# Kernel tuning notes

Hardware: AMD Instinct MI355X
Metric: run time of the kernel (lower is better)

## Reference

```python
import jax, jax.numpy as jnp
import numpy as np

LAMBDA_COORD = 5.0
LAMBDA_NOOBJ = 0.5
CELL_SILE = 1.0 / 7.0


def setup_inputs() -> dict:
    key = jax.random.key(0)
    k1, k2, k3 = jax.random.split(key, 3)
    B, S, C = 16384, 49, 30
    predictions = jax.random.normal(k1, (B, S, C), dtype=jnp.float32)
    targets = jax.random.uniform(k2, (B, S, C), dtype=jnp.float32)
    # confidence column must be exactly 0/1 for the equality masks in the loss
    obj = (jax.random.uniform(k3, (B, S)) < 0.3).astype(jnp.float32)
    targets = targets.at[:, :, 4].set(obj)
    return {"predictions": predictions, "targets": targets}


def reference(predictions, targets):
    # Flatten cells: row-major order matches torch boolean indexing order.
    p = predictions.reshape(-1, 30)  # [N, 30], N = B*49
    t = targets.reshape(-1, 30)
    conf = t[:, 4]
    coord_mask = conf == 1.0
    noobj = (conf == 0.0).astype(p.dtype)

    # no-object confidence loss on columns [4, 9]
    noobj_loss = LAMBDA_NOOBJ * jnp.sum(
        noobj * ((p[:, 4] - t[:, 4]) ** 2 + (p[:, 9] - t[:, 9]) ** 2))

    # The original zips N_obj rows against N_obj//2 output rows, so only the
    # first floor(N_obj/2) object cells (in flattened order) contribute.
    n_obj = jnp.sum(coord_mask.astype(jnp.int32))
    rank = jnp.cumsum(coord_mask.astype(jnp.int32))  # 1-indexed object rank
    w = (coord_mask & (rank <= n_obj // 2)).astype(p.dtype)

    # pred boxes: columns [0:4] and [5:9] -> [N, 2, 4]
    pb = p[:, :10].reshape(-1, 2, 5)[..., :4]
    # faithful in-place transform: a = xy*c - wh ; b = a*c + wh
    pa = pb[..., :2] * CELL_SILE - pb[..., 2:4]
    pbb = pa * CELL_SILE + pb[..., 2:4]
    pbox = jnp.concatenate([pa, pbb], axis=-1)  # [N, 2, 4]

    tb = jnp.square(t[:, :4])
    ta = tb[:, :2] * CELL_SILE - tb[:, 2:4]
    tbb = ta * CELL_SILE + tb[:, 2:4]
    tbox = jnp.concatenate([ta, tbb], axis=-1)  # [N, 4]

    # torchvision.ops.box_iou, batched over cells
    lt = jnp.maximum(pbox[..., :2], tbox[:, None, :2])
    rb = jnp.minimum(pbox[..., 2:], tbox[:, None, 2:])
    whd = jnp.clip(rb - lt, 0.0)
    inter = whd[..., 0] * whd[..., 1]  # [N, 2]
    area_p = (pbox[..., 2] - pbox[..., 0]) * (pbox[..., 3] - pbox[..., 1])
    area_t = (tbox[:, 2] - tbox[:, 0]) * (tbox[:, 3] - tbox[:, 1])
    iou = inter / (area_p + area_t[:, None] - inter)  # [N, 2]

    idx = jnp.argmax(iou, axis=1)  # responsible box per cell
    sel = jnp.take_along_axis(p[:, :10].reshape(-1, 2, 5),
                              idx[:, None, None], axis=1)[:, 0, :]  # [N, 5]
    obj_idx = jnp.argmax(t[:, 10:], axis=1)
    sel_cls = jnp.take_along_axis(p[:, 10:], obj_idx[:, None], axis=1)[:, 0]

    center = jnp.sum(w * jnp.sum((sel[:, :2] - t[:, :2]) ** 2, axis=1))
    xywh = jnp.sum(w * jnp.sum((sel[:, 2:4] - t[:, 2:4]) ** 2, axis=1))
    # original compares column 5 twice (confidence_loss and classier_loss are
    # the same term): pred class prob vs constant 1
    conf_l = jnp.sum(w * (sel_cls - 1.0) ** 2)
    cls_l = jnp.sum(w * (sel_cls - 1.0) ** 2)

    return LAMBDA_COORD * (center + xywh + conf_l + cls_l) + noobj_loss
```

## Files before the change

kernel.cpp:

```cpp
#include <hip/hip_runtime.h>


#define COLS 30
#define NB   3136

#define ROW_MATH_BODY                                                        \
    const float C = 1.0f / 7.0f;                                             \
    float conf = b2.x;                         \
    coord = (conf == 1.0f);                                                  \
    noo = 0.0f;                                                              \
    if (conf == 0.0f) {                                                      \
        float d4_ = a2.x - conf;                                             \
        float d9_ = a4.y - b4.y;                                             \
        noo = d4_ * d4_ + d9_ * d9_;                                         \
    }                                                                        \
    float T0 = b0.x, T1 = b0.y, T2v = b1.x, T3 = b1.y;                       \
    float tb0 = T0 * T0, tb1 = T1 * T1, tb2 = T2v * T2v, tb3 = T3 * T3;      \
    float tax = tb0 * C - tb2, tay = tb1 * C - tb3;                          \
    float tbx = tax * C + tb2, tby = tay * C + tb3;                          \
    float areaT = (tbx - tax) * (tby - tay);                                 \
    float pax0 = a0.x * C - a1.x, pay0 = a0.y * C - a1.y;                    \
    float pbx0 = pax0 * C + a1.x, pby0 = pay0 * C + a1.y;                    \
    float pax1 = a2.y * C - a3.y, pay1 = a3.x * C - a4.x;                    \
    float pbx1 = pax1 * C + a3.y, pby1 = pay1 * C + a4.x;                    \
    float ltx = fmaxf(pax0, tax), lty = fmaxf(pay0, tay);                    \
    float rbx = fminf(pbx0, tbx), rby = fminf(pby0, tby);                    \
    float wx = fmaxf(rbx - ltx, 0.0f), wy = fmaxf(rby - lty, 0.0f);          \
    float inter = wx * wy;                                                   \
    float areaP = (pbx0 - pax0) * (pby0 - pay0);                             \
    float iou0 = inter / (areaP + areaT - inter);                            \
    ltx = fmaxf(pax1, tax); lty = fmaxf(pay1, tay);                          \
    rbx = fminf(pbx1, tbx); rby = fminf(pby1, tby);                          \
    wx = fmaxf(rbx - ltx, 0.0f); wy = fmaxf(rby - lty, 0.0f);                \
    inter = wx * wy;                                                         \
    areaP = (pbx1 - pax1) * (pby1 - pay1);                                   \
    float iou1 = inter / (areaP + areaT - inter);                            \
    int idx = (iou1 > iou0) ? 1 : 0;              \
    float sx = idx ? a2.y : a0.x;                                            \
    float sy = idx ? a3.x : a0.y;                                            \
    float sw = idx ? a3.y : a1.x;                                            \
    float sh = idx ? a4.x : a1.y;                                            \
    float best = b5.x, pc = a5.x;                \
    CLS_STEP(b5.y,  a5.y)  CLS_STEP(b6.x,  a6.x)  CLS_STEP(b6.y,  a6.y)      \
    CLS_STEP(b7.x,  a7.x)  CLS_STEP(b7.y,  a7.y)  CLS_STEP(b8.x,  a8.x)      \
    CLS_STEP(b8.y,  a8.y)  CLS_STEP(b9.x,  a9.x)  CLS_STEP(b9.y,  a9.y)      \
    CLS_STEP(b10.x, a10.x) CLS_STEP(b10.y, a10.y) CLS_STEP(b11.x, a11.x)     \
    CLS_STEP(b11.y, a11.y) CLS_STEP(b12.x, a12.x) CLS_STEP(b12.y, a12.y)     \
    CLS_STEP(b13.x, a13.x) CLS_STEP(b13.y, a13.y) CLS_STEP(b14.x, a14.x)     \
    CLS_STEP(b14.y, a14.y)                                                   \
    float d0 = sx - T0, d1 = sy - T1, d2 = sw - T2v, d3 = sh - T3;           \
    float dc = pc - 1.0f;                                                    \
    r = d0 * d0 + d1 * d1 + d2 * d2 + d3 * d3 + 2.0f * dc * dc;

#define CLS_STEP(tv, pv) { float v_ = (tv); if (v_ > best) { best = v_; pc = (pv); } }

__device__ __forceinline__ void row_compute_vals(
    float2 a0, float2 a1, float2 a2, float2 a3, float2 a4,
    float2 a5, float2 a6, float2 a7, float2 a8, float2 a9,
    float2 a10, float2 a11, float2 a12, float2 a13, float2 a14,
    float2 b0, float2 b1, float2 b2, float2 b3, float2 b4,
    float2 b5, float2 b6, float2 b7, float2 b8, float2 b9,
    float2 b10, float2 b11, float2 b12, float2 b13, float2 b14,
    bool& coord, float& r, float& noo)
{
    ROW_MATH_BODY
}

__device__ __forceinline__ void row_load_compute(
    const float* __restrict__ gp, const float* __restrict__ gt, long row,
    bool& coord, float& r, float& noo)
{
    const float2* P2 = (const float2*)(gp + row * (long)COLS);
    const float2* T2 = (const float2*)(gt + row * (long)COLS);
    float2 a0 = P2[0],  a1 = P2[1],  a2 = P2[2],  a3 = P2[3],  a4 = P2[4];
    float2 a5 = P2[5],  a6 = P2[6],  a7 = P2[7],  a8 = P2[8],  a9 = P2[9];
    float2 a10 = P2[10], a11 = P2[11], a12 = P2[12], a13 = P2[13], a14 = P2[14];
    float2 b0 = T2[0],  b1 = T2[1],  b2 = T2[2],  b3 = T2[3],  b4 = T2[4];
    float2 b5 = T2[5],  b6 = T2[6],  b7 = T2[7],  b8 = T2[8],  b9 = T2[9];
    float2 b10 = T2[10], b11 = T2[11], b12 = T2[12], b13 = T2[13], b14 = T2[14];
    ROW_MATH_BODY
}

__global__ __launch_bounds__(256, 3) void yolo_k1(const float* __restrict__ gp,
                                                  const float* __restrict__ gt,
                                                  int* __restrict__ cnt,
                                                  float* __restrict__ sumR,
                                                  float* __restrict__ noo) {
    __shared__ float wr[4], wn[4];
    __shared__ int wc[4];
    int tid = threadIdx.x;
    long row = (long)blockIdx.x * 256 + tid;
    unsigned int voff = (unsigned int)(row * (long)(COLS * 4));

    float2 p0, p1, p2, p3, p4, p5, p6, p7, p8, p9, p10, p11, p12, p13, p14;
    float2 q0, q1, q2, q3, q4, q5, q6, q7, q8, q9, q10, q11, q12, q13, q14;
    asm volatile(
        "global_load_dwordx2 %0,  %[off], %[pb]\n\t"
        "global_load_dwordx2 %1,  %[off], %[pb] offset:8\n\t"
        "global_load_dwordx2 %2,  %[off], %[pb] offset:16\n\t"
        "global_load_dwordx2 %3,  %[off], %[pb] offset:24\n\t"
        "global_load_dwordx2 %4,  %[off], %[pb] offset:32\n\t"
        "global_load_dwordx2 %5,  %[off], %[pb] offset:40\n\t"
        "global_load_dwordx2 %6,  %[off], %[pb] offset:48\n\t"
        "global_load_dwordx2 %7,  %[off], %[pb] offset:56\n\t"
        "global_load_dwordx2 %8,  %[off], %[pb] offset:64\n\t"
        "global_load_dwordx2 %9,  %[off], %[pb] offset:72\n\t"
        "global_load_dwordx2 %10, %[off], %[pb] offset:80\n\t"
        "global_load_dwordx2 %11, %[off], %[pb] offset:88\n\t"
        "global_load_dwordx2 %12, %[off], %[pb] offset:96\n\t"
        "global_load_dwordx2 %13, %[off], %[pb] offset:104\n\t"
        "global_load_dwordx2 %14, %[off], %[pb] offset:112\n\t"
        "global_load_dwordx2 %15, %[off], %[tb]\n\t"
        "global_load_dwordx2 %16, %[off], %[tb] offset:8\n\t"
        "global_load_dwordx2 %17, %[off], %[tb] offset:16\n\t"
        "global_load_dwordx2 %18, %[off], %[tb] offset:24\n\t"
        "global_load_dwordx2 %19, %[off], %[tb] offset:32\n\t"
        "global_load_dwordx2 %20, %[off], %[tb] offset:40\n\t"
        "global_load_dwordx2 %21, %[off], %[tb] offset:48\n\t"
        "global_load_dwordx2 %22, %[off], %[tb] offset:56\n\t"
        "global_load_dwordx2 %23, %[off], %[tb] offset:64\n\t"
        "global_load_dwordx2 %24, %[off], %[tb] offset:72\n\t"
        "global_load_dwordx2 %25, %[off], %[tb] offset:80\n\t"
        "global_load_dwordx2 %26, %[off], %[tb] offset:88\n\t"
        "global_load_dwordx2 %27, %[off], %[tb] offset:96\n\t"
        "global_load_dwordx2 %28, %[off], %[tb] offset:104\n\t"
        "global_load_dwordx2 %29, %[off], %[tb] offset:112\n\t"
        "s_waitcnt vmcnt(0)"
        : "=v"(p0), "=v"(p1), "=v"(p2), "=v"(p3), "=v"(p4),
          "=v"(p5), "=v"(p6), "=v"(p7), "=v"(p8), "=v"(p9),
          "=v"(p10), "=v"(p11), "=v"(p12), "=v"(p13), "=v"(p14),
          "=v"(q0), "=v"(q1), "=v"(q2), "=v"(q3), "=v"(q4),
          "=v"(q5), "=v"(q6), "=v"(q7), "=v"(q8), "=v"(q9),
          "=v"(q10), "=v"(q11), "=v"(q12), "=v"(q13), "=v"(q14)
        : [off]"v"(voff), [pb]"s"(gp), [tb]"s"(gt)
        : "memory");

    bool coord; float r, nt;
    row_compute_vals(p0, p1, p2, p3, p4, p5, p6, p7, p8, p9,
                     p10, p11, p12, p13, p14,
                     q0, q1, q2, q3, q4, q5, q6, q7, q8, q9,
                     q10, q11, q12, q13, q14, coord, r, nt);
    float rl = coord ? r : 0.0f;

    unsigned long long bal = __ballot(coord);
    int c = (int)__popcll(bal);
#pragma unroll
    for (int off = 32; off > 0; off >>= 1) {
        rl += __shfl_down(rl, off);
        nt += __shfl_down(nt, off);
    }
    int wave = tid >> 6, lane = tid & 63;
    if (lane == 0) { wr[wave] = rl; wn[wave] = nt; wc[wave] = c; }
    __syncthreads();
    if (tid == 0) {
        cnt[blockIdx.x]  = wc[0] + wc[1] + wc[2] + wc[3];
        sumR[blockIdx.x] = wr[0] + wr[1] + wr[2] + wr[3];
        noo[blockIdx.x]  = wn[0] + wn[1] + wn[2] + wn[3];
    }
}

__global__ __launch_bounds__(256) void yolo_k2(const int* __restrict__ cnt,
                                               const float* __restrict__ sumR,
                                               const float* __restrict__ noo,
                                               const float* __restrict__ gp,
                                               const float* __restrict__ gt,
                                               float* __restrict__ out) {
    __shared__ int   wsum[4];
    __shared__ float wf[4], wn2[4];
    __shared__ int   s_bstar, s_kstar;
    __shared__ float s_base;
    __shared__ int   s_wcnt[4];
    int tid = threadIdx.x;
    int lane = tid & 63, wave = tid >> 6;
    if (tid == 0) { s_bstar = -1; s_kstar = 0; }

    const int PER = 13;
    int start = tid * PER;
    int end = min(NB, start + PER);

    int cloc = 0; float nloc = 0.0f;
    for (int i = start; i < end; ++i) { cloc += cnt[i]; nloc += noo[i]; }

    int incl = cloc;
#pragma unroll
    for (int off = 1; off < 64; off <<= 1) {
        int v = __shfl_up(incl, off);
        if (lane >= off) incl += v;
    }
    if (lane == 63) wsum[wave] = incl;
    __syncthreads();
    int woff = 0;
#pragma unroll
    for (int w = 0; w < 4; ++w) woff += (w < wave) ? wsum[w] : 0;
    int ex = woff + incl - cloc;
    int n_obj = wsum[0] + wsum[1] + wsum[2] + wsum[3];
    int n_half = n_obj >> 1;

    float acc = 0.0f;
    int running = ex;
    for (int i = start; i < end; ++i) {
        int ci = cnt[i];
        if (ci > 0) {
            if (running + ci <= n_half) {
                acc += sumR[i];
            } else if (running < n_half) {
                s_bstar = i;
                s_kstar = n_half - running;
            }
        }
        running += ci;
    }

#pragma unroll
    for (int off = 32; off > 0; off >>= 1) {
        acc  += __shfl_down(acc, off);
        nloc += __shfl_down(nloc, off);
    }
    if (lane == 0) { wf[wave] = acc; wn2[wave] = nloc; }
    __syncthreads();
    if (tid == 0)
        s_base = 5.0f * (wf[0] + wf[1] + wf[2] + wf[3])
               + 0.5f * (wn2[0] + wn2[1] + wn2[2] + wn2[3]);
    __syncthreads();

    int bstar = s_bstar, kstar = s_kstar;
    float total = 0.0f;
    if (bstar >= 0) {
        long row = (long)bstar * 256 + tid;
        bool coord; float r, nt;
        row_load_compute(gp, gt, row, coord, r, nt);
        unsigned long long bal = __ballot(coord);
        if (lane == 0) s_wcnt[wave] = (int)__popcll(bal);
        __syncthreads();
        int waveoff = 0;
#pragma unroll
        for (int w = 0; w < 4; ++w) waveoff += (w < wave) ? s_wcnt[w] : 0;
        unsigned long long below_incl =
            (lane == 63) ? bal : (bal & ((1ull << (lane + 1)) - 1ull));
        int rank = waveoff + (int)__popcll(below_incl);
        float val = (coord && rank <= kstar) ? r : 0.0f;
#pragma unroll
        for (int off = 32; off > 0; off >>= 1) val += __shfl_down(val, off);
        if (lane == 0) wf[wave] = val;
        __syncthreads();
        if (tid == 0) total = wf[0] + wf[1] + wf[2] + wf[3];
    }
    if (tid == 0) out[0] = s_base + 5.0f * total;
}

extern "C" void kernel_launch(void* const* d_in, const int* in_sizes, int n_in,
                              void* d_out, int out_size, void* d_ws, size_t ws_size,
                              hipStream_t stream) {
    (void)in_sizes; (void)n_in; (void)out_size; (void)ws_size;
    const float* p = (const float*)d_in[0];
    const float* t = (const float*)d_in[1];
    char* ws = (char*)d_ws;
    int*   cnt  = (int*)ws;
    float* sumR = (float*)(ws + (size_t)NB * 4);
    float* noo  = (float*)(ws + (size_t)NB * 8);
    float* out  = (float*)d_out;

    yolo_k1<<<NB, 256, 0, stream>>>(p, t, cnt, sumR, noo);
    yolo_k2<<<1, 256, 0, stream>>>(cnt, sumR, noo, p, t, out);
}
```

Baseline: 213.1 us.

## Process two rows per thread with dwordx4 loads and halve block count

Each thread in the first kernel now handles a pair of adjacent rows, loading them as 16-byte dwordx4 vectors instead of 8-byte loads, and the block count is halved. The second kernel's per-thread block-prefix loop and its boundary-block rank computation are changed to match the two-rows-per-thread ordering. This is meant to cut the number of memory instructions and the per-block reduction overhead. In exchange, registers per thread roughly double and the occupancy hint drops from 3 to 2, so less latency can be hidden.

```diff
diff --git a/kernel.cpp b/kernel.cpp
--- a/kernel.cpp
+++ b/kernel.cpp
@@ -2,7 +2,7 @@
 
 
 #define COLS 30
-#define NB   3136
+#define NB   1568
 
 #define ROW_MATH_BODY                                                        \
     const float C = 1.0f / 7.0f;                                             \
@@ -81,7 +81,9 @@
     ROW_MATH_BODY
 }
 
-__global__ __launch_bounds__(256, 3) void yolo_k1(const float* __restrict__ gp,
+#define F2(v, c0, c1) make_float2((v).c0, (v).c1)
+
+__global__ __launch_bounds__(256, 2) void yolo_k1(const float* __restrict__ gp,
                                                   const float* __restrict__ gt,
                                                   int* __restrict__ cnt,
                                                   float* __restrict__ sumR,
@@ -89,61 +91,71 @@
     __shared__ float wr[4], wn[4];
     __shared__ int wc[4];
     int tid = threadIdx.x;
-    long row = (long)blockIdx.x * 256 + tid;
-    unsigned int voff = (unsigned int)(row * (long)(COLS * 4));
-
-    float2 p0, p1, p2, p3, p4, p5, p6, p7, p8, p9, p10, p11, p12, p13, p14;
-    float2 q0, q1, q2, q3, q4, q5, q6, q7, q8, q9, q10, q11, q12, q13, q14;
+    long pair = (long)blockIdx.x * 256 + tid;
+    unsigned int voff = (unsigned int)(pair * 240l);
+
+    float4 f0, f1, f2, f3, f4, f5, f6, f7, f8, f9, f10, f11, f12, f13, f14;
+    float4 g0, g1, g2, g3, g4, g5, g6, g7, g8, g9, g10, g11, g12, g13, g14;
     asm volatile(
-        "global_load_dwordx2 %0,  %[off], %[pb]\n\t"
-        "global_load_dwordx2 %1,  %[off], %[pb] offset:8\n\t"
-        "global_load_dwordx2 %2,  %[off], %[pb] offset:16\n\t"
-        "global_load_dwordx2 %3,  %[off], %[pb] offset:24\n\t"
-        "global_load_dwordx2 %4,  %[off], %[pb] offset:32\n\t"
-        "global_load_dwordx2 %5,  %[off], %[pb] offset:40\n\t"
-        "global_load_dwordx2 %6,  %[off], %[pb] offset:48\n\t"
-        "global_load_dwordx2 %7,  %[off], %[pb] offset:56\n\t"
-        "global_load_dwordx2 %8,  %[off], %[pb] offset:64\n\t"
-        "global_load_dwordx2 %9,  %[off], %[pb] offset:72\n\t"
-        "global_load_dwordx2 %10, %[off], %[pb] offset:80\n\t"
-        "global_load_dwordx2 %11, %[off], %[pb] offset:88\n\t"
-        "global_load_dwordx2 %12, %[off], %[pb] offset:96\n\t"
-        "global_load_dwordx2 %13, %[off], %[pb] offset:104\n\t"
-        "global_load_dwordx2 %14, %[off], %[pb] offset:112\n\t"
-        "global_load_dwordx2 %15, %[off], %[tb]\n\t"
-        "global_load_dwordx2 %16, %[off], %[tb] offset:8\n\t"
-        "global_load_dwordx2 %17, %[off], %[tb] offset:16\n\t"
-        "global_load_dwordx2 %18, %[off], %[tb] offset:24\n\t"
-        "global_load_dwordx2 %19, %[off], %[tb] offset:32\n\t"
-        "global_load_dwordx2 %20, %[off], %[tb] offset:40\n\t"
-        "global_load_dwordx2 %21, %[off], %[tb] offset:48\n\t"
-        "global_load_dwordx2 %22, %[off], %[tb] offset:56\n\t"
-        "global_load_dwordx2 %23, %[off], %[tb] offset:64\n\t"
-        "global_load_dwordx2 %24, %[off], %[tb] offset:72\n\t"
-        "global_load_dwordx2 %25, %[off], %[tb] offset:80\n\t"
-        "global_load_dwordx2 %26, %[off], %[tb] offset:88\n\t"
-        "global_load_dwordx2 %27, %[off], %[tb] offset:96\n\t"
-        "global_load_dwordx2 %28, %[off], %[tb] offset:104\n\t"
-        "global_load_dwordx2 %29, %[off], %[tb] offset:112\n\t"
+        "global_load_dwordx4 %0,  %[off], %[pb]\n\t"
+        "global_load_dwordx4 %1,  %[off], %[pb] offset:16\n\t"
+        "global_load_dwordx4 %2,  %[off], %[pb] offset:32\n\t"
+        "global_load_dwordx4 %3,  %[off], %[pb] offset:48\n\t"
+        "global_load_dwordx4 %4,  %[off], %[pb] offset:64\n\t"
+        "global_load_dwordx4 %5,  %[off], %[pb] offset:80\n\t"
+        "global_load_dwordx4 %6,  %[off], %[pb] offset:96\n\t"
+        "global_load_dwordx4 %7,  %[off], %[pb] offset:112\n\t"
+        "global_load_dwordx4 %8,  %[off], %[pb] offset:128\n\t"
+        "global_load_dwordx4 %9,  %[off], %[pb] offset:144\n\t"
+        "global_load_dwordx4 %10, %[off], %[pb] offset:160\n\t"
+        "global_load_dwordx4 %11, %[off], %[pb] offset:176\n\t"
+        "global_load_dwordx4 %12, %[off], %[pb] offset:192\n\t"
+        "global_load_dwordx4 %13, %[off], %[pb] offset:208\n\t"
+        "global_load_dwordx4 %14, %[off], %[pb] offset:224\n\t"
+        "global_load_dwordx4 %15, %[off], %[tb]\n\t"
+        "global_load_dwordx4 %16, %[off], %[tb] offset:16\n\t"
+        "global_load_dwordx4 %17, %[off], %[tb] offset:32\n\t"
+        "global_load_dwordx4 %18, %[off], %[tb] offset:48\n\t"
+        "global_load_dwordx4 %19, %[off], %[tb] offset:64\n\t"
+        "global_load_dwordx4 %20, %[off], %[tb] offset:80\n\t"
+        "global_load_dwordx4 %21, %[off], %[tb] offset:96\n\t"
+        "global_load_dwordx4 %22, %[off], %[tb] offset:112\n\t"
+        "global_load_dwordx4 %23, %[off], %[tb] offset:128\n\t"
+        "global_load_dwordx4 %24, %[off], %[tb] offset:144\n\t"
+        "global_load_dwordx4 %25, %[off], %[tb] offset:160\n\t"
+        "global_load_dwordx4 %26, %[off], %[tb] offset:176\n\t"
+        "global_load_dwordx4 %27, %[off], %[tb] offset:192\n\t"
+        "global_load_dwordx4 %28, %[off], %[tb] offset:208\n\t"
+        "global_load_dwordx4 %29, %[off], %[tb] offset:224\n\t"
         "s_waitcnt vmcnt(0)"
-        : "=v"(p0), "=v"(p1), "=v"(p2), "=v"(p3), "=v"(p4),
-          "=v"(p5), "=v"(p6), "=v"(p7), "=v"(p8), "=v"(p9),
-          "=v"(p10), "=v"(p11), "=v"(p12), "=v"(p13), "=v"(p14),
-          "=v"(q0), "=v"(q1), "=v"(q2), "=v"(q3), "=v"(q4),
-          "=v"(q5), "=v"(q6), "=v"(q7), "=v"(q8), "=v"(q9),
-          "=v"(q10), "=v"(q11), "=v"(q12), "=v"(q13), "=v"(q14)
+        : "=v"(f0), "=v"(f1), "=v"(f2), "=v"(f3), "=v"(f4),
+          "=v"(f5), "=v"(f6), "=v"(f7), "=v"(f8), "=v"(f9),
+          "=v"(f10), "=v"(f11), "=v"(f12), "=v"(f13), "=v"(f14),
+          "=v"(g0), "=v"(g1), "=v"(g2), "=v"(g3), "=v"(g4),
+          "=v"(g5), "=v"(g6), "=v"(g7), "=v"(g8), "=v"(g9),
+          "=v"(g10), "=v"(g11), "=v"(g12), "=v"(g13), "=v"(g14)
         : [off]"v"(voff), [pb]"s"(gp), [tb]"s"(gt)
         : "memory");
 
-    bool coord; float r, nt;
-    row_compute_vals(p0, p1, p2, p3, p4, p5, p6, p7, p8, p9,
-                     p10, p11, p12, p13, p14,
-                     q0, q1, q2, q3, q4, q5, q6, q7, q8, q9,
-                     q10, q11, q12, q13, q14, coord, r, nt);
-    float rl = coord ? r : 0.0f;
-
-    unsigned long long bal = __ballot(coord);
-    int c = (int)__popcll(bal);
+    bool cA, cB; float rA, rB, nA, nB;
+    row_compute_vals(F2(f0,x,y), F2(f0,z,w), F2(f1,x,y), F2(f1,z,w), F2(f2,x,y),
+                     F2(f2,z,w), F2(f3,x,y), F2(f3,z,w), F2(f4,x,y), F2(f4,z,w),
+                     F2(f5,x,y), F2(f5,z,w), F2(f6,x,y), F2(f6,z,w), F2(f7,x,y),
+                     F2(g0,x,y), F2(g0,z,w), F2(g1,x,y), F2(g1,z,w), F2(g2,x,y),
+                     F2(g2,z,w), F2(g3,x,y), F2(g3,z,w), F2(g4,x,y), F2(g4,z,w),
+                     F2(g5,x,y), F2(g5,z,w), F2(g6,x,y), F2(g6,z,w), F2(g7,x,y),
+                     cA, rA, nA);
+    row_compute_vals(F2(f7,z,w), F2(f8,x,y), F2(f8,z,w), F2(f9,x,y), F2(f9,z,w),
+                     F2(f10,x,y), F2(f10,z,w), F2(f11,x,y), F2(f11,z,w), F2(f12,x,y),
+                     F2(f12,z,w), F2(f13,x,y), F2(f13,z,w), F2(f14,x,y), F2(f14,z,w),
+                     F2(g7,z,w), F2(g8,x,y), F2(g8,z,w), F2(g9,x,y), F2(g9,z,w),
+                     F2(g10,x,y), F2(g10,z,w), F2(g11,x,y), F2(g11,z,w), F2(g12,x,y),
+                     F2(g12,z,w), F2(g13,x,y), F2(g13,z,w), F2(g14,x,y), F2(g14,z,w),
+                     cB, rB, nB);
+
+    float rl = (cA ? rA : 0.0f) + (cB ? rB : 0.0f);
+    float nt = nA + nB;
+    int c = (int)__popcll(__ballot(cA)) + (int)__popcll(__ballot(cB));
 #pragma unroll
     for (int off = 32; off > 0; off >>= 1) {
         rl += __shfl_down(rl, off);
@@ -174,7 +186,7 @@
     int lane = tid & 63, wave = tid >> 6;
     if (tid == 0) { s_bstar = -1; s_kstar = 0; }
 
-    const int PER = 13;
+    const int PER = 7;
     int start = tid * PER;
     int end = min(NB, start + PER);
 
@@ -226,19 +238,27 @@
     int bstar = s_bstar, kstar = s_kstar;
     float total = 0.0f;
     if (bstar >= 0) {
-        long row = (long)bstar * 256 + tid;
-        bool coord; float r, nt;
-        row_load_compute(gp, gt, row, coord, r, nt);
-        unsigned long long bal = __ballot(coord);
-        if (lane == 0) s_wcnt[wave] = (int)__popcll(bal);
+        long rowA = (long)bstar * 512 + 2 * tid;
+        bool cA, cB; float rA, rB, nA, nB;
+        row_load_compute(gp, gt, rowA, cA, rA, nA);
+        row_load_compute(gp, gt, rowA + 1, cB, rB, nB);
+        unsigned long long balA = __ballot(cA);
+        unsigned long long balB = __ballot(cB);
+        if (lane == 0)
+            s_wcnt[wave] = (int)__popcll(balA) + (int)__popcll(balB);
         __syncthreads();
         int waveoff = 0;
 #pragma unroll
         for (int w = 0; w < 4; ++w) waveoff += (w < wave) ? s_wcnt[w] : 0;
-        unsigned long long below_incl =
-            (lane == 63) ? bal : (bal & ((1ull << (lane + 1)) - 1ull));
-        int rank = waveoff + (int)__popcll(below_incl);
-        float val = (coord && rank <= kstar) ? r : 0.0f;
+        unsigned long long lemask =
+            (lane == 63) ? ~0ull : ((1ull << (lane + 1)) - 1ull);
+        unsigned long long ltmask = (1ull << lane) - 1ull;
+        int rankA = waveoff + (int)__popcll(balA & lemask)
+                            + (int)__popcll(balB & ltmask);
+        int rankB = waveoff + (int)__popcll(balA & lemask)
+                            + (int)__popcll(balB & lemask);
+        float val = ((cA && rankA <= kstar) ? rA : 0.0f)
+                  + ((cB && rankB <= kstar) ? rB : 0.0f);
 #pragma unroll
         for (int off = 32; off > 0; off >>= 1) val += __shfl_down(val, off);
         if (lane == 0) wf[wave] = val;
```

New measurement: 214.9 us. No clear change (+0.9%).

## Stage row tiles into LDS via global_load_lds with single-wave 128-row blocks

Applied to the files above, without the earlier changes.

Replaces the per-thread strided dwordx2 global loads (120-byte row stride per lane) with coalesced 16-byte global_load_lds transfers that stage a 128-row tile of predictions and targets into LDS. Each single-wave block then computes two rows per thread from LDS. Per-tile counts and sums are packed into one float4 in the workspace, and the finalize kernel reads those packed stats. The aim is fully coalesced DRAM access without going through registers. The cost is twice as many tiles for the serial finalize kernel to scan, plus LDS bank conflicts from the 30-float row stride when rows are read back.

```diff
diff --git a/kernel.cpp b/kernel.cpp
--- a/kernel.cpp
+++ b/kernel.cpp
@@ -2,7 +2,9 @@
 
 
 #define COLS 30
-#define NB   3136
+#define TROWS 128
+#define TBYTES (TROWS * COLS * 4)
+#define NT 6272
 
 #define ROW_MATH_BODY                                                        \
     const float C = 1.0f / 7.0f;                                             \
@@ -54,24 +56,11 @@
 
 #define CLS_STEP(tv, pv) { float v_ = (tv); if (v_ > best) { best = v_; pc = (pv); } }
 
-__device__ __forceinline__ void row_compute_vals(
-    float2 a0, float2 a1, float2 a2, float2 a3, float2 a4,
-    float2 a5, float2 a6, float2 a7, float2 a8, float2 a9,
-    float2 a10, float2 a11, float2 a12, float2 a13, float2 a14,
-    float2 b0, float2 b1, float2 b2, float2 b3, float2 b4,
-    float2 b5, float2 b6, float2 b7, float2 b8, float2 b9,
-    float2 b10, float2 b11, float2 b12, float2 b13, float2 b14,
-    bool& coord, float& r, float& noo)
+__device__ __forceinline__ void row_compute_ptr(
+    const float* P, const float* T, bool& coord, float& r, float& noo)
 {
-    ROW_MATH_BODY
-}
-
-__device__ __forceinline__ void row_load_compute(
-    const float* __restrict__ gp, const float* __restrict__ gt, long row,
-    bool& coord, float& r, float& noo)
-{
-    const float2* P2 = (const float2*)(gp + row * (long)COLS);
-    const float2* T2 = (const float2*)(gt + row * (long)COLS);
+    const float2* P2 = (const float2*)P;
+    const float2* T2 = (const float2*)T;
     float2 a0 = P2[0],  a1 = P2[1],  a2 = P2[2],  a3 = P2[3],  a4 = P2[4];
     float2 a5 = P2[5],  a6 = P2[6],  a7 = P2[7],  a8 = P2[8],  a9 = P2[9];
     float2 a10 = P2[10], a11 = P2[11], a12 = P2[12], a13 = P2[13], a14 = P2[14];
@@ -81,87 +70,47 @@
     ROW_MATH_BODY
 }
 
-__global__ __launch_bounds__(256, 3) void yolo_k1(const float* __restrict__ gp,
-                                                  const float* __restrict__ gt,
-                                                  int* __restrict__ cnt,
-                                                  float* __restrict__ sumR,
-                                                  float* __restrict__ noo) {
-    __shared__ float wr[4], wn[4];
-    __shared__ int wc[4];
+__global__ __launch_bounds__(64) void yolo_k1(const float* __restrict__ gp,
+                                              const float* __restrict__ gt,
+                                              float4* __restrict__ stats) {
+    __shared__ float lds[2 * TROWS * COLS];
     int tid = threadIdx.x;
-    long row = (long)blockIdx.x * 256 + tid;
-    unsigned int voff = (unsigned int)(row * (long)(COLS * 4));
-
-    float2 p0, p1, p2, p3, p4, p5, p6, p7, p8, p9, p10, p11, p12, p13, p14;
-    float2 q0, q1, q2, q3, q4, q5, q6, q7, q8, q9, q10, q11, q12, q13, q14;
-    asm volatile(
-        "global_load_dwordx2 %0,  %[off], %[pb]\n\t"
-        "global_load_dwordx2 %1,  %[off], %[pb] offset:8\n\t"
-        "global_load_dwordx2 %2,  %[off], %[pb] offset:16\n\t"
-        "global_load_dwordx2 %3,  %[off], %[pb] offset:24\n\t"
-        "global_load_dwordx2 %4,  %[off], %[pb] offset:32\n\t"
-        "global_load_dwordx2 %5,  %[off], %[pb] offset:40\n\t"
-        "global_load_dwordx2 %6,  %[off], %[pb] offset:48\n\t"
-        "global_load_dwordx2 %7,  %[off], %[pb] offset:56\n\t"
-        "global_load_dwordx2 %8,  %[off], %[pb] offset:64\n\t"
-        "global_load_dwordx2 %9,  %[off], %[pb] offset:72\n\t"
-        "global_load_dwordx2 %10, %[off], %[pb] offset:80\n\t"
-        "global_load_dwordx2 %11, %[off], %[pb] offset:88\n\t"
-        "global_load_dwordx2 %12, %[off], %[pb] offset:96\n\t"
-        "global_load_dwordx2 %13, %[off], %[pb] offset:104\n\t"
-        "global_load_dwordx2 %14, %[off], %[pb] offset:112\n\t"
-        "global_load_dwordx2 %15, %[off], %[tb]\n\t"
-        "global_load_dwordx2 %16, %[off], %[tb] offset:8\n\t"
-        "global_load_dwordx2 %17, %[off], %[tb] offset:16\n\t"
-        "global_load_dwordx2 %18, %[off], %[tb] offset:24\n\t"
-        "global_load_dwordx2 %19, %[off], %[tb] offset:32\n\t"
-        "global_load_dwordx2 %20, %[off], %[tb] offset:40\n\t"
-        "global_load_dwordx2 %21, %[off], %[tb] offset:48\n\t"
-        "global_load_dwordx2 %22, %[off], %[tb] offset:56\n\t"
-        "global_load_dwordx2 %23, %[off], %[tb] offset:64\n\t"
-        "global_load_dwordx2 %24, %[off], %[tb] offset:72\n\t"
-        "global_load_dwordx2 %25, %[off], %[tb] offset:80\n\t"
-        "global_load_dwordx2 %26, %[off], %[tb] offset:88\n\t"
-        "global_load_dwordx2 %27, %[off], %[tb] offset:96\n\t"
-        "global_load_dwordx2 %28, %[off], %[tb] offset:104\n\t"
-        "global_load_dwordx2 %29, %[off], %[tb] offset:112\n\t"
-        "s_waitcnt vmcnt(0)"
-        : "=v"(p0), "=v"(p1), "=v"(p2), "=v"(p3), "=v"(p4),
-          "=v"(p5), "=v"(p6), "=v"(p7), "=v"(p8), "=v"(p9),
-          "=v"(p10), "=v"(p11), "=v"(p12), "=v"(p13), "=v"(p14),
-          "=v"(q0), "=v"(q1), "=v"(q2), "=v"(q3), "=v"(q4),
-          "=v"(q5), "=v"(q6), "=v"(q7), "=v"(q8), "=v"(q9),
-          "=v"(q10), "=v"(q11), "=v"(q12), "=v"(q13), "=v"(q14)
-        : [off]"v"(voff), [pb]"s"(gp), [tb]"s"(gt)
-        : "memory");
-
-    bool coord; float r, nt;
-    row_compute_vals(p0, p1, p2, p3, p4, p5, p6, p7, p8, p9,
-                     p10, p11, p12, p13, p14,
-                     q0, q1, q2, q3, q4, q5, q6, q7, q8, q9,
-                     q10, q11, q12, q13, q14, coord, r, nt);
-    float rl = coord ? r : 0.0f;
-
-    unsigned long long bal = __ballot(coord);
-    int c = (int)__popcll(bal);
+    long tile = blockIdx.x;
+    const char* gpb = (const char*)gp + tile * (long)TBYTES;
+    const char* gtb = (const char*)gt + tile * (long)TBYTES;
+    char* lb = (char*)lds;
+#pragma unroll
+    for (int k = 0; k < 15; ++k) {
+        int off = k * 1024 + tid * 16;
+        __builtin_amdgcn_global_load_lds(
+            (const __attribute__((address_space(1))) void*)(gpb + off),
+            (__attribute__((address_space(3))) void*)(lb + k * 1024), 16, 0, 0);
+    }
+#pragma unroll
+    for (int k = 0; k < 15; ++k) {
+        int off = k * 1024 + tid * 16;
+        __builtin_amdgcn_global_load_lds(
+            (const __attribute__((address_space(1))) void*)(gtb + off),
+            (__attribute__((address_space(3))) void*)(lb + TBYTES + k * 1024), 16, 0, 0);
+    }
+
+    const float* lp = lds;
+    const float* lt = lds + TROWS * COLS;
+    bool cA, cB; float rA, rB, nA, nB;
+    row_compute_ptr(lp + tid * COLS, lt + tid * COLS, cA, rA, nA);
+    row_compute_ptr(lp + (tid + 64) * COLS, lt + (tid + 64) * COLS, cB, rB, nB);
+    float rl = (cA ? rA : 0.0f) + (cB ? rB : 0.0f);
+    float nn = nA + nB;
+    int c = (int)__popcll(__ballot(cA)) + (int)__popcll(__ballot(cB));
 #pragma unroll
     for (int off = 32; off > 0; off >>= 1) {
         rl += __shfl_down(rl, off);
-        nt += __shfl_down(nt, off);
-    }
-    int wave = tid >> 6, lane = tid & 63;
-    if (lane == 0) { wr[wave] = rl; wn[wave] = nt; wc[wave] = c; }
-    __syncthreads();
-    if (tid == 0) {
-        cnt[blockIdx.x]  = wc[0] + wc[1] + wc[2] + wc[3];
-        sumR[blockIdx.x] = wr[0] + wr[1] + wr[2] + wr[3];
-        noo[blockIdx.x]  = wn[0] + wn[1] + wn[2] + wn[3];
-    }
-}
-
-__global__ __launch_bounds__(256) void yolo_k2(const int* __restrict__ cnt,
-                                               const float* __restrict__ sumR,
-                                               const float* __restrict__ noo,
+        nn += __shfl_down(nn, off);
+    }
+    if (tid == 0) stats[tile] = make_float4((float)c, rl, nn, 0.0f);
+}
+
+__global__ __launch_bounds__(256) void yolo_k2(const float4* __restrict__ stats,
                                                const float* __restrict__ gp,
                                                const float* __restrict__ gt,
                                                float* __restrict__ out) {
@@ -174,12 +123,15 @@
     int lane = tid & 63, wave = tid >> 6;
     if (tid == 0) { s_bstar = -1; s_kstar = 0; }
 
-    const int PER = 13;
+    const int PER = 25;
     int start = tid * PER;
-    int end = min(NB, start + PER);
+    int end = min(NT, start + PER);
 
     int cloc = 0; float nloc = 0.0f;
-    for (int i = start; i < end; ++i) { cloc += cnt[i]; nloc += noo[i]; }
+    for (int i = start; i < end; ++i) {
+        float4 s = stats[i];
+        cloc += (int)s.x; nloc += s.z;
+    }
 
     int incl = cloc;
 #pragma unroll
@@ -199,10 +151,11 @@
     float acc = 0.0f;
     int running = ex;
     for (int i = start; i < end; ++i) {
-        int ci = cnt[i];
+        float4 s = stats[i];
+        int ci = (int)s.x;
         if (ci > 0) {
             if (running + ci <= n_half) {
-                acc += sumR[i];
+                acc += s.y;
             } else if (running < n_half) {
                 s_bstar = i;
                 s_kstar = n_half - running;
@@ -226,9 +179,13 @@
     int bstar = s_bstar, kstar = s_kstar;
     float total = 0.0f;
     if (bstar >= 0) {
-        long row = (long)bstar * 256 + tid;
-        bool coord; float r, nt;
-        row_load_compute(gp, gt, row, coord, r, nt);
+        bool coord = false; float r = 0.0f;
+        if (tid < TROWS) {
+            long row = (long)bstar * TROWS + tid;
+            float nthrow;
+            row_compute_ptr(gp + row * (long)COLS, gt + row * (long)COLS,
+                            coord, r, nthrow);
+        }
         unsigned long long bal = __ballot(coord);
         if (lane == 0) s_wcnt[wave] = (int)__popcll(bal);
         __syncthreads();
@@ -254,12 +211,9 @@
     (void)in_sizes; (void)n_in; (void)out_size; (void)ws_size;
     const float* p = (const float*)d_in[0];
     const float* t = (const float*)d_in[1];
-    char* ws = (char*)d_ws;
-    int*   cnt  = (int*)ws;
-    float* sumR = (float*)(ws + (size_t)NB * 4);
-    float* noo  = (float*)(ws + (size_t)NB * 8);
-    float* out  = (float*)d_out;
-
-    yolo_k1<<<NB, 256, 0, stream>>>(p, t, cnt, sumR, noo);
-    yolo_k2<<<1, 256, 0, stream>>>(cnt, sumR, noo, p, t, out);
-}
+    float4* stats = (float4*)d_ws;
+    float* out = (float*)d_out;
+
+    yolo_k1<<<NT, 64, 0, stream>>>(p, t, stats);
+    yolo_k2<<<1, 256, 0, stream>>>(stats, p, t, out);
+}
```

Measured after the change: 216.2 us. No clear change (+1.5%).
